# Performance work log

Measured on AMD Instinct MI355X. Metric: run time of the kernel, lower is better.

Reference implementation:

```python
import math
import jax, jax.numpy as jnp
import numpy as np

N, T, D, H = 256, 128, 1024, 1024


def setup_inputs() -> dict:
    key = jax.random.key(0)
    k1, k2, k3, k4, k5 = jax.random.split(key, 5)
    x = jax.random.normal(k1, (N, T, D), dtype=jnp.float32)
    A = jax.random.normal(k2, (N, H, 4, 4), dtype=jnp.float32)
    Wx = jax.random.normal(k3, (D, 4 * H), dtype=jnp.float32) / math.sqrt(D)
    Wh = jax.random.normal(k4, (H, 4 * H), dtype=jnp.float32) / math.sqrt(H)
    Wattn = jax.random.normal(k5, (H, 4 * H), dtype=jnp.float32) / math.sqrt(H)
    b = jnp.zeros((4 * H,), dtype=jnp.float32)
    return {"x": x, "A": A, "Wx": Wx, "Wh": Wh, "Wattn": Wattn, "b": b}


def reference(x, A, Wx, Wh, Wattn, b):
    n, t, d = x.shape
    h = A.shape[1]
    A_flat = A.reshape(n, h, -1)            # (N, H, 16)
    h0 = A_flat.mean(axis=-1)               # mean over 4x4 grid
    c0 = h0
    scale = 1.0 / math.sqrt(h)

    def step(carry, xt):
        prev_h, prev_c = carry
        # scaled dot-product attention over the 16 spatial locations
        scores = jnp.einsum('nh,nhl->nl', prev_h, A_flat) * scale  # (N, 16)
        w = jax.nn.softmax(scores, axis=1)
        attn = jnp.einsum('nhl,nl->nh', A_flat, w)                 # (N, H)
        pre = xt @ Wx + prev_h @ Wh + attn @ Wattn + b             # (N, 4H)
        ai, af, ao, ag = jnp.split(pre, 4, axis=1)
        i = jax.nn.sigmoid(ai)
        f = jax.nn.sigmoid(af)
        o = jax.nn.sigmoid(ao)
        g = jnp.tanh(ag)
        next_c = f * prev_c + i * g
        next_h = o * jnp.tanh(next_c)
        return (next_h, next_c), next_h

    xs = jnp.swapaxes(x, 0, 1)               # (T, N, D)
    _, hs = jax.lax.scan(step, (h0, c0), xs)  # hs: (T, N, H)
    return jnp.swapaxes(hs, 0, 1)             # (N, T, H)
```

## Files before the change

kernel.cpp:

```cpp
#include <hip/hip_runtime.h>
#include <hip/hip_bf16.h>
#include <stdint.h>

#define N_ 256
#define T_ 128
#define D_ 1024
#define H_ 1024
#define FH_ 4096
#define K2_ 2048

typedef __bf16 bf16x8 __attribute__((ext_vector_type(8)));
typedef float f32x4 __attribute__((ext_vector_type(4)));

__global__ __launch_bounds__(256) void transpose_cast(
    const float* __restrict__ src, int cols,
    __hip_bfloat16* __restrict__ dst, int dst_stride, int dst_coloff)
{
    __shared__ float tile[32][33];
    int cb = blockIdx.x * 32, rb = blockIdx.y * 32;
    int tx = threadIdx.x, ty = threadIdx.y;
#pragma unroll
    for (int i = 0; i < 4; i++)
        tile[ty + i * 8][tx] = src[(size_t)(rb + ty + i * 8) * cols + cb + tx];
    __syncthreads();
#pragma unroll
    for (int i = 0; i < 4; i++)
        dst[(size_t)(cb + ty + i * 8) * dst_stride + dst_coloff + rb + tx] =
            __float2bfloat16(tile[tx][ty + i * 8]);
}

#define BM 64
#define BN 128
#define BK 64
#define BKP 72

__global__ __launch_bounds__(256) void gemm_x(
    const float* __restrict__ Xf,
    const __hip_bfloat16* __restrict__ BT,
    __hip_bfloat16* __restrict__ Cp, int t0)
{
    __shared__ __hip_bfloat16 Al[BM][BKP];
    __shared__ __hip_bfloat16 Bl[BN][BKP];
    const int tid = threadIdx.x;
    const int lane = tid & 63, wid = tid >> 6;
    const int m0 = blockIdx.y * BM, n0 = blockIdx.x * BN;
    const int wm = (wid >> 1) * 32, wn = (wid & 1) * 64;
    const int rs = tid >> 3, kc = (tid & 7) * 8;
    f32x4 acc[2][4] = {};

    for (int k0 = 0; k0 < D_; k0 += BK) {
#pragma unroll
        for (int p = 0; p < BM; p += 32) {
            int r = rs + p;
            int g = m0 + r;
            int nn = g & 255, tl = g >> 8;
            const float* s = Xf + ((size_t)nn * T_ + (t0 + tl)) * D_ + k0 + kc;
            float4 v0 = *reinterpret_cast<const float4*>(s);
            float4 v1 = *reinterpret_cast<const float4*>(s + 4);
            __hip_bfloat16 h8[8];
            h8[0] = __float2bfloat16(v0.x); h8[1] = __float2bfloat16(v0.y);
            h8[2] = __float2bfloat16(v0.z); h8[3] = __float2bfloat16(v0.w);
            h8[4] = __float2bfloat16(v1.x); h8[5] = __float2bfloat16(v1.y);
            h8[6] = __float2bfloat16(v1.z); h8[7] = __float2bfloat16(v1.w);
            *reinterpret_cast<int4*>(&Al[r][kc]) = *reinterpret_cast<const int4*>(h8);
        }
#pragma unroll
        for (int p = 0; p < BN; p += 32) {
            int r = rs + p;
            const __hip_bfloat16* s = BT + (size_t)(n0 + r) * D_ + k0 + kc;
            *reinterpret_cast<int4*>(&Bl[r][kc]) = *reinterpret_cast<const int4*>(s);
        }
        __syncthreads();
        const int ko = (lane >> 4) * 8;
#pragma unroll
        for (int kk = 0; kk < BK; kk += 32) {
            bf16x8 a0 = *reinterpret_cast<const bf16x8*>(&Al[wm + (lane & 15)][kk + ko]);
            bf16x8 a1 = *reinterpret_cast<const bf16x8*>(&Al[wm + 16 + (lane & 15)][kk + ko]);
#pragma unroll
            for (int ni = 0; ni < 4; ni++) {
                bf16x8 bq = *reinterpret_cast<const bf16x8*>(&Bl[wn + ni * 16 + (lane & 15)][kk + ko]);
                acc[0][ni] = __builtin_amdgcn_mfma_f32_16x16x32_bf16(a0, bq, acc[0][ni], 0, 0, 0);
                acc[1][ni] = __builtin_amdgcn_mfma_f32_16x16x32_bf16(a1, bq, acc[1][ni], 0, 0, 0);
            }
        }
        __syncthreads();
    }
    const int cr = (lane >> 4) * 4, ccol = lane & 15;
#pragma unroll
    for (int mi = 0; mi < 2; mi++)
#pragma unroll
        for (int ni = 0; ni < 4; ni++)
#pragma unroll
            for (int r = 0; r < 4; r++) {
                size_t idx = (size_t)(m0 + wm + mi * 16 + cr + r) * FH_ + (n0 + wn + ni * 16 + ccol);
                Cp[idx] = __float2bfloat16(acc[mi][ni][r]);
            }
}

__global__ __launch_bounds__(256) void abf_cast(
    const float* __restrict__ A, __hip_bfloat16* __restrict__ Abf)
{
    size_t i = ((size_t)blockIdx.x * 256 + threadIdx.x) * 4;
    float4 v = *reinterpret_cast<const float4*>(A + i);
    __hip_bfloat16 o[4];
    o[0] = __float2bfloat16(v.x); o[1] = __float2bfloat16(v.y);
    o[2] = __float2bfloat16(v.z); o[3] = __float2bfloat16(v.w);
    *reinterpret_cast<uint2*>(Abf + i) = *reinterpret_cast<uint2*>(o);
}

__global__ __launch_bounds__(256) void init_p(
    const float* __restrict__ A, float* __restrict__ cbuf,
    __hip_bfloat16* __restrict__ hb0)
{
    const int n = blockIdx.x, tid = threadIdx.x;
    float hv[4];
#pragma unroll
    for (int q = 0; q < 4; q++) {
        const float4* Ap = reinterpret_cast<const float4*>(A + ((size_t)n * H_ + tid * 4 + q) * 16);
        float4 q0 = Ap[0], q1 = Ap[1], q2 = Ap[2], q3 = Ap[3];
        float s = q0.x + q0.y + q0.z + q0.w + q1.x + q1.y + q1.z + q1.w
                + q2.x + q2.y + q2.z + q2.w + q3.x + q3.y + q3.z + q3.w;
        hv[q] = s * 0.0625f;
    }
    *reinterpret_cast<float4*>(cbuf + (size_t)n * H_ + tid * 4) = *reinterpret_cast<float4*>(hv);
    __hip_bfloat16 h4[4];
#pragma unroll
    for (int q = 0; q < 4; q++) h4[q] = __float2bfloat16(hv[q]);
    *reinterpret_cast<uint2*>(hb0 + (size_t)n * K2_ + tid * 4) = *reinterpret_cast<uint2*>(h4);
}

__global__ __launch_bounds__(256) void wattn2(
    __hip_bfloat16* __restrict__ hbt,
    const __hip_bfloat16* __restrict__ Abf)
{
    __shared__ float red[4][16];
    const int n = blockIdx.x, tid = threadIdx.x;
    const int lane = tid & 63, wv4 = tid >> 6;

    float h4[4];
    {
        uint2 hraw = *reinterpret_cast<const uint2*>(hbt + (size_t)n * K2_ + tid * 4);
        __hip_bfloat16 hb4[4];
        *reinterpret_cast<uint2*>(hb4) = hraw;
#pragma unroll
        for (int q = 0; q < 4; q++) h4[q] = __bfloat162float(hb4[q]);
    }
    bf16x8 a[4][2];
    const __hip_bfloat16* ap = Abf + ((size_t)n * H_ + tid * 4) * 16;
#pragma unroll
    for (int q = 0; q < 4; q++) {
        a[q][0] = *reinterpret_cast<const bf16x8*>(ap + q * 16);
        a[q][1] = *reinterpret_cast<const bf16x8*>(ap + q * 16 + 8);
    }
    float spv[16];
#pragma unroll
    for (int l = 0; l < 8; l++) {
        spv[l]     = h4[0] * (float)a[0][0][l] + h4[1] * (float)a[1][0][l]
                   + h4[2] * (float)a[2][0][l] + h4[3] * (float)a[3][0][l];
        spv[l + 8] = h4[0] * (float)a[0][1][l] + h4[1] * (float)a[1][1][l]
                   + h4[2] * (float)a[2][1][l] + h4[3] * (float)a[3][1][l];
    }
#pragma unroll
    for (int l = 0; l < 16; l++) {
        spv[l] += __shfl_xor(spv[l], 1);  spv[l] += __shfl_xor(spv[l], 2);
        spv[l] += __shfl_xor(spv[l], 4);  spv[l] += __shfl_xor(spv[l], 8);
        spv[l] += __shfl_xor(spv[l], 16); spv[l] += __shfl_xor(spv[l], 32);
    }
    if (lane == 0) {
#pragma unroll
        for (int l = 0; l < 16; l++) red[wv4][l] = spv[l];
    }
    __syncthreads();
    float w[16], se = 0.f;
    {
        float sc[16], m;
#pragma unroll
        for (int l = 0; l < 16; l++)
            sc[l] = (red[0][l] + red[1][l] + red[2][l] + red[3][l]) * 0.03125f;
        m = sc[0];
#pragma unroll
        for (int l = 1; l < 16; l++) m = fmaxf(m, sc[l]);
#pragma unroll
        for (int l = 0; l < 16; l++) { w[l] = __expf(sc[l] - m); se += w[l]; }
        float inv = 1.f / se;
#pragma unroll
        for (int l = 0; l < 16; l++) w[l] *= inv;
    }
    __hip_bfloat16 o4[4];
#pragma unroll
    for (int q = 0; q < 4; q++) {
        float s = 0.f;
#pragma unroll
        for (int l = 0; l < 8; l++) s += w[l] * (float)a[q][0][l];
#pragma unroll
        for (int l = 0; l < 8; l++) s += w[l + 8] * (float)a[q][1][l];
        o4[q] = __float2bfloat16(s);
    }
    *reinterpret_cast<uint2*>(hbt + (size_t)n * K2_ + H_ + tid * 4) =
        *reinterpret_cast<uint2*>(o4);
}

#define LDAp 136

__global__ __launch_bounds__(512) void step_gemm(
    const __hip_bfloat16* __restrict__ hb_in,
    __hip_bfloat16* __restrict__ hb_out,
    const __hip_bfloat16* __restrict__ W2T,
    const __hip_bfloat16* __restrict__ xp,
    const float* __restrict__ bias,
    float* __restrict__ cbuf,
    float* __restrict__ out, int t)
{
    __shared__ __align__(16) char smem[69632];
    float* pls = (float*)smem;

    const int tid = threadIdx.x;
    const int lane = tid & 63, wv = tid >> 6;
    const int bid = blockIdx.x;
    const int q = bid >> 3;
    const int ct = (bid & 7) + 8 * (q >> 2);
    const int r  = q & 3;
    const int hc0 = ct * 16, n0 = r * 64;
    const int rs = tid >> 4;
    const int kc = (tid & 15) * 8;
    const int l15 = lane & 15, ko8 = (lane >> 4) * 8;
    const int wm = (wv >> 1) * 16, wn = (wv & 1) * 32;

    const int gB0 = ((rs) >> 4) * 1024 + hc0 + (rs & 15);
    const int gB1 = ((rs + 32) >> 4) * 1024 + hc0 + ((rs + 32) & 15);
    const __hip_bfloat16* aS0 = hb_in + (size_t)(n0 + rs) * K2_ + kc;
    const __hip_bfloat16* aS1 = hb_in + (size_t)(n0 + rs + 32) * K2_ + kc;
    const __hip_bfloat16* bS0 = W2T + (size_t)gB0 * K2_ + kc;
    const __hip_bfloat16* bS1 = W2T + (size_t)gB1 * K2_ + kc;

    int4 ra0, ra1, rb0, rb1;
    auto LOAD = [&](int k0) {
        ra0 = *reinterpret_cast<const int4*>(aS0 + k0);
        ra1 = *reinterpret_cast<const int4*>(aS1 + k0);
        rb0 = *reinterpret_cast<const int4*>(bS0 + k0);
        rb1 = *reinterpret_cast<const int4*>(bS1 + k0);
    };
    auto WRITE = [&](int b) {
        __hip_bfloat16* Al = (__hip_bfloat16*)(smem + b * 17408);
        __hip_bfloat16* Bl = (__hip_bfloat16*)(smem + 34816 + b * 17408);
        *reinterpret_cast<int4*>(Al + rs * LDAp + kc) = ra0;
        *reinterpret_cast<int4*>(Al + (rs + 32) * LDAp + kc) = ra1;
        *reinterpret_cast<int4*>(Bl + rs * LDAp + kc) = rb0;
        *reinterpret_cast<int4*>(Bl + (rs + 32) * LDAp + kc) = rb1;
    };

    LOAD(0);
    WRITE(0);
    __syncthreads();

    f32x4 acc0{}, acc1{};
#pragma unroll 1
    for (int it = 0; it < 16; ++it) {
        if (it < 15) LOAD((it + 1) * 128);
        const int cur = it & 1;
        const __hip_bfloat16* pA  = (const __hip_bfloat16*)(smem + cur * 17408) + (wm + l15) * LDAp + ko8;
        const __hip_bfloat16* pB0 = (const __hip_bfloat16*)(smem + 34816 + cur * 17408) + (wn + l15) * LDAp + ko8;
        const __hip_bfloat16* pB1 = pB0 + 16 * LDAp;
#pragma unroll
        for (int kf = 0; kf < 4; kf++) {
            bf16x8 af = *reinterpret_cast<const bf16x8*>(pA + kf * 32);
            bf16x8 b0 = *reinterpret_cast<const bf16x8*>(pB0 + kf * 32);
            bf16x8 b1 = *reinterpret_cast<const bf16x8*>(pB1 + kf * 32);
            acc0 = __builtin_amdgcn_mfma_f32_16x16x32_bf16(af, b0, acc0, 0, 0, 0);
            acc1 = __builtin_amdgcn_mfma_f32_16x16x32_bf16(af, b1, acc1, 0, 0, 0);
        }
        __syncthreads();
        if (it < 15) {
            WRITE(cur ^ 1);
            __syncthreads();
        }
    }

    {
        const int cr = (lane >> 4) * 4;
#pragma unroll
        for (int r4 = 0; r4 < 4; r4++) {
            pls[(wm + cr + r4) * 68 + wn + l15]      = acc0[r4];
            pls[(wm + cr + r4) * 68 + wn + 16 + l15] = acc1[r4];
        }
    }
    __syncthreads();

    {
        const int n_l = tid >> 3, c2 = (tid & 7) * 2;
        const int nn = n0 + n_l;
        float hv2[2], cv2[2];
        const size_t cbase = (size_t)nn * H_ + hc0 + c2;
        float2 cold = *reinterpret_cast<const float2*>(cbuf + cbase);
        cv2[0] = cold.x; cv2[1] = cold.y;
#pragma unroll
        for (int cc = 0; cc < 2; cc++) {
            const int c = c2 + cc;
            float pre[4];
#pragma unroll
            for (int s = 0; s < 4; s++) {
                const int gj = s * 1024 + hc0 + c;
                pre[s] = pls[n_l * 68 + s * 16 + c]
                       + __bfloat162float(xp[(size_t)nn * FH_ + gj]) + bias[gj];
            }
            float iv = 1.f / (1.f + __expf(-pre[0]));
            float fv = 1.f / (1.f + __expf(-pre[1]));
            float ov = 1.f / (1.f + __expf(-pre[2]));
            float gx = fminf(fmaxf(pre[3], -20.f), 20.f);
            float eg = __expf(2.f * gx);
            float gv = (eg - 1.f) / (eg + 1.f);
            float c2v = fv * cv2[cc] + iv * gv;
            cv2[cc] = c2v;
            float cx = fminf(fmaxf(c2v, -20.f), 20.f);
            float ec = __expf(2.f * cx);
            hv2[cc] = ov * (ec - 1.f) / (ec + 1.f);
        }
        *reinterpret_cast<float2*>(cbuf + cbase) = make_float2(cv2[0], cv2[1]);
        *reinterpret_cast<float2*>(out + ((size_t)nn * T_ + t) * H_ + hc0 + c2) =
            make_float2(hv2[0], hv2[1]);
        __hip_bfloat16 h2[2];
        h2[0] = __float2bfloat16(hv2[0]);
        h2[1] = __float2bfloat16(hv2[1]);
        *reinterpret_cast<uint32_t*>(hb_out + (size_t)nn * K2_ + hc0 + c2) =
            *reinterpret_cast<uint32_t*>(h2);
    }
}

extern "C" void kernel_launch(void* const* d_in, const int* in_sizes, int n_in,
                              void* d_out, int out_size, void* d_ws, size_t ws_size,
                              hipStream_t stream)
{
    const float* x     = (const float*)d_in[0];
    const float* A     = (const float*)d_in[1];
    const float* Wx    = (const float*)d_in[2];
    const float* Wh    = (const float*)d_in[3];
    const float* Wattn = (const float*)d_in[4];
    const float* b     = (const float*)d_in[5];
    float* out = (float*)d_out;
    char* ws = (char*)d_ws;
    dim3 tb(32, 8);

    const size_t SZ_W2T = (size_t)FH_ * K2_ * 2;
    const size_t SZ_WxT = (size_t)FH_ * D_ * 2;
    const size_t SZ_Abf = (size_t)N_ * H_ * 16 * 2;
    const size_t SZ_HB  = (size_t)N_ * K2_ * 2;
    const size_t SZ_C   = (size_t)N_ * H_ * 4;
    const size_t SZ_XPT = (size_t)N_ * FH_ * 2;

    size_t off = 0;
    __hip_bfloat16* W2T = (__hip_bfloat16*)(ws + off); off += SZ_W2T;
    __hip_bfloat16* WxT = (__hip_bfloat16*)(ws + off); off += SZ_WxT;
    __hip_bfloat16* Abf = (__hip_bfloat16*)(ws + off); off += SZ_Abf;
    __hip_bfloat16* hbA = (__hip_bfloat16*)(ws + off); off += SZ_HB;
    __hip_bfloat16* hbB = (__hip_bfloat16*)(ws + off); off += SZ_HB;
    float* cbuf = (float*)(ws + off); off += SZ_C;
    __hip_bfloat16* xpb = (__hip_bfloat16*)(ws + off);

    size_t rem = (ws_size > off) ? (ws_size - off) : 0;
    int TC = 64;
    while (TC > 1 && (size_t)TC * SZ_XPT > rem) TC >>= 1;

    transpose_cast<<<dim3(FH_ / 32, H_ / 32), tb, 0, stream>>>(Wh, FH_, W2T, K2_, 0);
    transpose_cast<<<dim3(FH_ / 32, H_ / 32), tb, 0, stream>>>(Wattn, FH_, W2T, K2_, H_);
    transpose_cast<<<dim3(FH_ / 32, D_ / 32), tb, 0, stream>>>(Wx, FH_, WxT, D_, 0);
    abf_cast<<<dim3((N_ * H_ * 16) / 1024), 256, 0, stream>>>(A, Abf);
    init_p<<<N_, 256, 0, stream>>>(A, cbuf, hbA);

    __hip_bfloat16* hbp[2] = {hbA, hbB};
    for (int t0 = 0; t0 < T_; t0 += TC) {
        int tc = (T_ - t0 < TC) ? (T_ - t0) : TC;
        gemm_x<<<dim3(FH_ / BN, tc * N_ / BM), 256, 0, stream>>>(x, WxT, xpb, t0);
        for (int tl = 0; tl < tc; tl++) {
            int t = t0 + tl;
            wattn2<<<N_, 256, 0, stream>>>(hbp[t & 1], Abf);
            step_gemm<<<dim3(256), 512, 0, stream>>>(
                hbp[t & 1], hbp[(t + 1) & 1], W2T,
                xpb + (size_t)tl * N_ * FH_, b, cbuf, out, t);
        }
    }
}
```

Before: 3.113 ms.

## Fuse attention and step GEMM into persistent kernel with grid barriers

Replaces the per-timestep pair of launches (attention kernel plus step GEMM) with one persistent kernel per time chunk. Blocks run the attention for one batch row, sync through a two-level atomic grid barrier, do the recurrent GEMM and LSTM update, then barrier again. The cell state stays in registers across steps, and the input-projection GEMM gets a remapped block order. This targets launch overhead and the DRAM round trip of c, at the cost of spin-wait barriers that need all 256 blocks co-resident, and a fixed chunk of 32 steps.

```diff
diff --git a/kernel.cpp b/kernel.cpp
--- a/kernel.cpp
+++ b/kernel.cpp
@@ -8,6 +8,7 @@
 #define H_ 1024
 #define FH_ 4096
 #define K2_ 2048
+#define TCHUNK 32
 
 typedef __bf16 bf16x8 __attribute__((ext_vector_type(8)));
 typedef float f32x4 __attribute__((ext_vector_type(4)));
@@ -43,7 +44,10 @@
     __shared__ __hip_bfloat16 Bl[BN][BKP];
     const int tid = threadIdx.x;
     const int lane = tid & 63, wid = tid >> 6;
-    const int m0 = blockIdx.y * BM, n0 = blockIdx.x * BN;
+    const int lin = blockIdx.y * gridDim.x + blockIdx.x;
+    const int cti = (lin & 7) + 8 * ((lin >> 3) & 3);
+    const int mti = lin >> 5;
+    const int m0 = mti * BM, n0 = cti * BN;
     const int wm = (wid >> 1) * 32, wn = (wid & 1) * 64;
     const int rs = tid >> 3, kc = (tid & 7) * 8;
     f32x4 acc[2][4] = {};
@@ -110,9 +114,10 @@
 
 __global__ __launch_bounds__(256) void init_p(
     const float* __restrict__ A, float* __restrict__ cbuf,
-    __hip_bfloat16* __restrict__ hb0)
+    __hip_bfloat16* __restrict__ hb0, unsigned* __restrict__ bar)
 {
     const int n = blockIdx.x, tid = threadIdx.x;
+    if (n == 0) { bar[tid] = 0u; bar[256 + tid] = 0u; }
     float hv[4];
 #pragma unroll
     for (int q = 0; q < 4; q++) {
@@ -129,94 +134,49 @@
     *reinterpret_cast<uint2*>(hb0 + (size_t)n * K2_ + tid * 4) = *reinterpret_cast<uint2*>(h4);
 }
 
-__global__ __launch_bounds__(256) void wattn2(
-    __hip_bfloat16* __restrict__ hbt,
-    const __hip_bfloat16* __restrict__ Abf)
-{
-    __shared__ float red[4][16];
-    const int n = blockIdx.x, tid = threadIdx.x;
-    const int lane = tid & 63, wv4 = tid >> 6;
-
-    float h4[4];
-    {
-        uint2 hraw = *reinterpret_cast<const uint2*>(hbt + (size_t)n * K2_ + tid * 4);
-        __hip_bfloat16 hb4[4];
-        *reinterpret_cast<uint2*>(hb4) = hraw;
-#pragma unroll
-        for (int q = 0; q < 4; q++) h4[q] = __bfloat162float(hb4[q]);
-    }
-    bf16x8 a[4][2];
-    const __hip_bfloat16* ap = Abf + ((size_t)n * H_ + tid * 4) * 16;
-#pragma unroll
-    for (int q = 0; q < 4; q++) {
-        a[q][0] = *reinterpret_cast<const bf16x8*>(ap + q * 16);
-        a[q][1] = *reinterpret_cast<const bf16x8*>(ap + q * 16 + 8);
-    }
-    float spv[16];
-#pragma unroll
-    for (int l = 0; l < 8; l++) {
-        spv[l]     = h4[0] * (float)a[0][0][l] + h4[1] * (float)a[1][0][l]
-                   + h4[2] * (float)a[2][0][l] + h4[3] * (float)a[3][0][l];
-        spv[l + 8] = h4[0] * (float)a[0][1][l] + h4[1] * (float)a[1][1][l]
-                   + h4[2] * (float)a[2][1][l] + h4[3] * (float)a[3][1][l];
-    }
-#pragma unroll
-    for (int l = 0; l < 16; l++) {
-        spv[l] += __shfl_xor(spv[l], 1);  spv[l] += __shfl_xor(spv[l], 2);
-        spv[l] += __shfl_xor(spv[l], 4);  spv[l] += __shfl_xor(spv[l], 8);
-        spv[l] += __shfl_xor(spv[l], 16); spv[l] += __shfl_xor(spv[l], 32);
-    }
-    if (lane == 0) {
-#pragma unroll
-        for (int l = 0; l < 16; l++) red[wv4][l] = spv[l];
+__device__ __forceinline__ void gridbar(unsigned* bar, int g)
+{
+    __syncthreads();
+    if (threadIdx.x == 0) {
+        __threadfence();
+        unsigned* leaf = bar + (g & 7) * 32;
+        unsigned* root = bar + 8 * 32;
+        unsigned* gen  = bar + 8 * 32 + 32;
+        unsigned tl = __hip_atomic_fetch_add(leaf, 1u, __ATOMIC_ACQ_REL, __HIP_MEMORY_SCOPE_AGENT);
+        unsigned r = tl >> 5;
+        if ((tl & 31u) == 31u) {
+            unsigned tr = __hip_atomic_fetch_add(root, 1u, __ATOMIC_ACQ_REL, __HIP_MEMORY_SCOPE_AGENT);
+            if ((tr & 7u) == 7u)
+                __hip_atomic_store(gen, r + 1u, __ATOMIC_RELEASE, __HIP_MEMORY_SCOPE_AGENT);
+        }
+        while (__hip_atomic_load(gen, __ATOMIC_ACQUIRE, __HIP_MEMORY_SCOPE_AGENT) < r + 1u)
+            __builtin_amdgcn_s_sleep(1);
+        __threadfence();
     }
     __syncthreads();
-    float w[16], se = 0.f;
-    {
-        float sc[16], m;
-#pragma unroll
-        for (int l = 0; l < 16; l++)
-            sc[l] = (red[0][l] + red[1][l] + red[2][l] + red[3][l]) * 0.03125f;
-        m = sc[0];
-#pragma unroll
-        for (int l = 1; l < 16; l++) m = fmaxf(m, sc[l]);
-#pragma unroll
-        for (int l = 0; l < 16; l++) { w[l] = __expf(sc[l] - m); se += w[l]; }
-        float inv = 1.f / se;
-#pragma unroll
-        for (int l = 0; l < 16; l++) w[l] *= inv;
-    }
-    __hip_bfloat16 o4[4];
-#pragma unroll
-    for (int q = 0; q < 4; q++) {
-        float s = 0.f;
-#pragma unroll
-        for (int l = 0; l < 8; l++) s += w[l] * (float)a[q][0][l];
-#pragma unroll
-        for (int l = 0; l < 8; l++) s += w[l + 8] * (float)a[q][1][l];
-        o4[q] = __float2bfloat16(s);
-    }
-    *reinterpret_cast<uint2*>(hbt + (size_t)n * K2_ + H_ + tid * 4) =
-        *reinterpret_cast<uint2*>(o4);
 }
 
 #define LDAp 136
 
-__global__ __launch_bounds__(512) void step_gemm(
-    const __hip_bfloat16* __restrict__ hb_in,
-    __hip_bfloat16* __restrict__ hb_out,
+__global__ __launch_bounds__(512) void persist3(
     const __hip_bfloat16* __restrict__ W2T,
-    const __hip_bfloat16* __restrict__ xp,
+    __hip_bfloat16* __restrict__ hbA,
+    __hip_bfloat16* __restrict__ hbB,
+    const __hip_bfloat16* __restrict__ xpb,
     const float* __restrict__ bias,
+    const __hip_bfloat16* __restrict__ Abf,
     float* __restrict__ cbuf,
-    float* __restrict__ out, int t)
-{
-    __shared__ __align__(16) char smem[69632];
+    float* __restrict__ out,
+    unsigned* __restrict__ bar,
+    int t0, int t1)
+{
+    __shared__ __align__(16) char smem[86016];
     float* pls = (float*)smem;
 
     const int tid = threadIdx.x;
     const int lane = tid & 63, wv = tid >> 6;
     const int bid = blockIdx.x;
+
     const int q = bid >> 3;
     const int ct = (bid & 7) + 8 * (q >> 2);
     const int r  = q & 3;
@@ -225,105 +185,176 @@
     const int kc = (tid & 15) * 8;
     const int l15 = lane & 15, ko8 = (lane >> 4) * 8;
     const int wm = (wv >> 1) * 16, wn = (wv & 1) * 32;
-
     const int gB0 = ((rs) >> 4) * 1024 + hc0 + (rs & 15);
     const int gB1 = ((rs + 32) >> 4) * 1024 + hc0 + ((rs + 32) & 15);
-    const __hip_bfloat16* aS0 = hb_in + (size_t)(n0 + rs) * K2_ + kc;
-    const __hip_bfloat16* aS1 = hb_in + (size_t)(n0 + rs + 32) * K2_ + kc;
     const __hip_bfloat16* bS0 = W2T + (size_t)gB0 * K2_ + kc;
     const __hip_bfloat16* bS1 = W2T + (size_t)gB1 * K2_ + kc;
 
-    int4 ra0, ra1, rb0, rb1;
-    auto LOAD = [&](int k0) {
-        ra0 = *reinterpret_cast<const int4*>(aS0 + k0);
-        ra1 = *reinterpret_cast<const int4*>(aS1 + k0);
-        rb0 = *reinterpret_cast<const int4*>(bS0 + k0);
-        rb1 = *reinterpret_cast<const int4*>(bS1 + k0);
-    };
-    auto WRITE = [&](int b) {
-        __hip_bfloat16* Al = (__hip_bfloat16*)(smem + b * 17408);
-        __hip_bfloat16* Bl = (__hip_bfloat16*)(smem + 34816 + b * 17408);
-        *reinterpret_cast<int4*>(Al + rs * LDAp + kc) = ra0;
-        *reinterpret_cast<int4*>(Al + (rs + 32) * LDAp + kc) = ra1;
-        *reinterpret_cast<int4*>(Bl + rs * LDAp + kc) = rb0;
-        *reinterpret_cast<int4*>(Bl + (rs + 32) * LDAp + kc) = rb1;
-    };
-
-    LOAD(0);
-    WRITE(0);
-    __syncthreads();
-
-    f32x4 acc0{}, acc1{};
+    const int n_l = tid >> 3, c2 = (tid & 7) * 2;
+    const int nn = n0 + n_l;
+    const size_t cbase = (size_t)nn * H_ + hc0 + c2;
+    float2 creg = *reinterpret_cast<const float2*>(cbuf + cbase);
+
+    for (int t = t0; t < t1; ++t) {
+        __hip_bfloat16* hcur = (t & 1) ? hbB : hbA;
+        __hip_bfloat16* hnxt = (t & 1) ? hbA : hbB;
+
+        {
+            float* red = (float*)smem;
+            float* wl  = (float*)smem + 128;
+            const int nA = bid;
+            uint32_t hraw = *reinterpret_cast<const uint32_t*>(
+                hcur + (size_t)nA * K2_ + tid * 2);
+            __hip_bfloat16 h2b[2];
+            *reinterpret_cast<uint32_t*>(h2b) = hraw;
+            float h0 = __bfloat162float(h2b[0]);
+            float h1 = __bfloat162float(h2b[1]);
+            const __hip_bfloat16* ap = Abf + ((size_t)nA * H_ + tid * 2) * 16;
+            bf16x8 a00 = *reinterpret_cast<const bf16x8*>(ap);
+            bf16x8 a01 = *reinterpret_cast<const bf16x8*>(ap + 8);
+            bf16x8 a10 = *reinterpret_cast<const bf16x8*>(ap + 16);
+            bf16x8 a11 = *reinterpret_cast<const bf16x8*>(ap + 24);
+            float spv[16];
+#pragma unroll
+            for (int l = 0; l < 8; l++) {
+                spv[l]     = h0 * (float)a00[l] + h1 * (float)a10[l];
+                spv[l + 8] = h0 * (float)a01[l] + h1 * (float)a11[l];
+            }
+#pragma unroll
+            for (int l = 0; l < 16; l++) {
+                spv[l] += __shfl_xor(spv[l], 1);  spv[l] += __shfl_xor(spv[l], 2);
+                spv[l] += __shfl_xor(spv[l], 4);  spv[l] += __shfl_xor(spv[l], 8);
+                spv[l] += __shfl_xor(spv[l], 16); spv[l] += __shfl_xor(spv[l], 32);
+            }
+            if (lane == 0) {
+#pragma unroll
+                for (int l = 0; l < 16; l++) red[wv * 16 + l] = spv[l];
+            }
+            __syncthreads();
+            if (tid < 16) {
+                float s = 0.f;
+#pragma unroll
+                for (int w8 = 0; w8 < 8; w8++) s += red[w8 * 16 + tid];
+                s *= 0.03125f;
+                float m = s;
+                m = fmaxf(m, __shfl_xor(m, 8)); m = fmaxf(m, __shfl_xor(m, 4));
+                m = fmaxf(m, __shfl_xor(m, 2)); m = fmaxf(m, __shfl_xor(m, 1));
+                float e = __expf(s - m);
+                float se = e;
+                se += __shfl_xor(se, 8); se += __shfl_xor(se, 4);
+                se += __shfl_xor(se, 2); se += __shfl_xor(se, 1);
+                wl[tid] = e / se;
+            }
+            __syncthreads();
+            float w[16];
+#pragma unroll
+            for (int l = 0; l < 16; l++) w[l] = wl[l];
+            float s0 = 0.f, s1 = 0.f;
+#pragma unroll
+            for (int l = 0; l < 8; l++) {
+                s0 += w[l] * (float)a00[l];  s0 += w[l + 8] * (float)a01[l];
+                s1 += w[l] * (float)a10[l];  s1 += w[l + 8] * (float)a11[l];
+            }
+            __hip_bfloat16 at2[2];
+            at2[0] = __float2bfloat16(s0);
+            at2[1] = __float2bfloat16(s1);
+            *reinterpret_cast<uint32_t*>(hcur + (size_t)nA * K2_ + H_ + tid * 2) =
+                *reinterpret_cast<uint32_t*>(at2);
+        }
+        gridbar(bar, bid);
+
+        const __hip_bfloat16* aS0 = hcur + (size_t)(n0 + rs) * K2_ + kc;
+        const __hip_bfloat16* aS1 = hcur + (size_t)(n0 + rs + 32) * K2_ + kc;
+        int4 ra0, ra1, rb0, rb1;
+        auto LOAD = [&](int k0) {
+            ra0 = *reinterpret_cast<const int4*>(aS0 + k0);
+            ra1 = *reinterpret_cast<const int4*>(aS1 + k0);
+            rb0 = *reinterpret_cast<const int4*>(bS0 + k0);
+            rb1 = *reinterpret_cast<const int4*>(bS1 + k0);
+        };
+        auto WRITE = [&](int b) {
+            __hip_bfloat16* Al = (__hip_bfloat16*)(smem + b * 17408);
+            __hip_bfloat16* Bl = (__hip_bfloat16*)(smem + 34816 + b * 17408);
+            *reinterpret_cast<int4*>(Al + rs * LDAp + kc) = ra0;
+            *reinterpret_cast<int4*>(Al + (rs + 32) * LDAp + kc) = ra1;
+            *reinterpret_cast<int4*>(Bl + rs * LDAp + kc) = rb0;
+            *reinterpret_cast<int4*>(Bl + (rs + 32) * LDAp + kc) = rb1;
+        };
+
+        LOAD(0);
+        WRITE(0);
+        __syncthreads();
+
+        f32x4 acc0{}, acc1{};
 #pragma unroll 1
-    for (int it = 0; it < 16; ++it) {
-        if (it < 15) LOAD((it + 1) * 128);
-        const int cur = it & 1;
-        const __hip_bfloat16* pA  = (const __hip_bfloat16*)(smem + cur * 17408) + (wm + l15) * LDAp + ko8;
-        const __hip_bfloat16* pB0 = (const __hip_bfloat16*)(smem + 34816 + cur * 17408) + (wn + l15) * LDAp + ko8;
-        const __hip_bfloat16* pB1 = pB0 + 16 * LDAp;
-#pragma unroll
-        for (int kf = 0; kf < 4; kf++) {
-            bf16x8 af = *reinterpret_cast<const bf16x8*>(pA + kf * 32);
-            bf16x8 b0 = *reinterpret_cast<const bf16x8*>(pB0 + kf * 32);
-            bf16x8 b1 = *reinterpret_cast<const bf16x8*>(pB1 + kf * 32);
-            acc0 = __builtin_amdgcn_mfma_f32_16x16x32_bf16(af, b0, acc0, 0, 0, 0);
-            acc1 = __builtin_amdgcn_mfma_f32_16x16x32_bf16(af, b1, acc1, 0, 0, 0);
+        for (int it = 0; it < 16; ++it) {
+            if (it < 15) LOAD((it + 1) * 128);
+            const int cur = it & 1;
+            const __hip_bfloat16* pA  = (const __hip_bfloat16*)(smem + cur * 17408) + (wm + l15) * LDAp + ko8;
+            const __hip_bfloat16* pB0 = (const __hip_bfloat16*)(smem + 34816 + cur * 17408) + (wn + l15) * LDAp + ko8;
+            const __hip_bfloat16* pB1 = pB0 + 16 * LDAp;
+#pragma unroll
+            for (int kf = 0; kf < 4; kf++) {
+                bf16x8 af = *reinterpret_cast<const bf16x8*>(pA + kf * 32);
+                bf16x8 b0 = *reinterpret_cast<const bf16x8*>(pB0 + kf * 32);
+                bf16x8 b1 = *reinterpret_cast<const bf16x8*>(pB1 + kf * 32);
+                acc0 = __builtin_amdgcn_mfma_f32_16x16x32_bf16(af, b0, acc0, 0, 0, 0);
+                acc1 = __builtin_amdgcn_mfma_f32_16x16x32_bf16(af, b1, acc1, 0, 0, 0);
+            }
+            __syncthreads();
+            if (it < 15) {
+                WRITE(cur ^ 1);
+                __syncthreads();
+            }
+        }
+
+        {
+            const int cr = (lane >> 4) * 4;
+#pragma unroll
+            for (int r4 = 0; r4 < 4; r4++) {
+                pls[(wm + cr + r4) * 68 + wn + l15]      = acc0[r4];
+                pls[(wm + cr + r4) * 68 + wn + 16 + l15] = acc1[r4];
+            }
         }
         __syncthreads();
-        if (it < 15) {
-            WRITE(cur ^ 1);
-            __syncthreads();
-        }
+
+        {
+            const __hip_bfloat16* xp = xpb + (size_t)(t - t0) * N_ * FH_;
+            float hv2[2], cv2[2] = {creg.x, creg.y};
+#pragma unroll
+            for (int cc = 0; cc < 2; cc++) {
+                const int c = c2 + cc;
+                float pre[4];
+#pragma unroll
+                for (int s = 0; s < 4; s++) {
+                    const int gj = s * 1024 + hc0 + c;
+                    pre[s] = pls[n_l * 68 + s * 16 + c]
+                           + __bfloat162float(xp[(size_t)nn * FH_ + gj]) + bias[gj];
+                }
+                float iv = 1.f / (1.f + __expf(-pre[0]));
+                float fv = 1.f / (1.f + __expf(-pre[1]));
+                float ov = 1.f / (1.f + __expf(-pre[2]));
+                float gx = fminf(fmaxf(pre[3], -20.f), 20.f);
+                float eg = __expf(2.f * gx);
+                float gv = (eg - 1.f) / (eg + 1.f);
+                float c2v = fv * cv2[cc] + iv * gv;
+                cv2[cc] = c2v;
+                float cx = fminf(fmaxf(c2v, -20.f), 20.f);
+                float ec = __expf(2.f * cx);
+                hv2[cc] = ov * (ec - 1.f) / (ec + 1.f);
+            }
+            creg = make_float2(cv2[0], cv2[1]);
+            *reinterpret_cast<float2*>(out + ((size_t)nn * T_ + t) * H_ + hc0 + c2) =
+                make_float2(hv2[0], hv2[1]);
+            __hip_bfloat16 h2[2];
+            h2[0] = __float2bfloat16(hv2[0]);
+            h2[1] = __float2bfloat16(hv2[1]);
+            *reinterpret_cast<uint32_t*>(hnxt + (size_t)nn * K2_ + hc0 + c2) =
+                *reinterpret_cast<uint32_t*>(h2);
+        }
+        gridbar(bar, bid);
     }
-
-    {
-        const int cr = (lane >> 4) * 4;
-#pragma unroll
-        for (int r4 = 0; r4 < 4; r4++) {
-            pls[(wm + cr + r4) * 68 + wn + l15]      = acc0[r4];
-            pls[(wm + cr + r4) * 68 + wn + 16 + l15] = acc1[r4];
-        }
-    }
-    __syncthreads();
-
-    {
-        const int n_l = tid >> 3, c2 = (tid & 7) * 2;
-        const int nn = n0 + n_l;
-        float hv2[2], cv2[2];
-        const size_t cbase = (size_t)nn * H_ + hc0 + c2;
-        float2 cold = *reinterpret_cast<const float2*>(cbuf + cbase);
-        cv2[0] = cold.x; cv2[1] = cold.y;
-#pragma unroll
-        for (int cc = 0; cc < 2; cc++) {
-            const int c = c2 + cc;
-            float pre[4];
-#pragma unroll
-            for (int s = 0; s < 4; s++) {
-                const int gj = s * 1024 + hc0 + c;
-                pre[s] = pls[n_l * 68 + s * 16 + c]
-                       + __bfloat162float(xp[(size_t)nn * FH_ + gj]) + bias[gj];
-            }
-            float iv = 1.f / (1.f + __expf(-pre[0]));
-            float fv = 1.f / (1.f + __expf(-pre[1]));
-            float ov = 1.f / (1.f + __expf(-pre[2]));
-            float gx = fminf(fmaxf(pre[3], -20.f), 20.f);
-            float eg = __expf(2.f * gx);
-            float gv = (eg - 1.f) / (eg + 1.f);
-            float c2v = fv * cv2[cc] + iv * gv;
-            cv2[cc] = c2v;
-            float cx = fminf(fmaxf(c2v, -20.f), 20.f);
-            float ec = __expf(2.f * cx);
-            hv2[cc] = ov * (ec - 1.f) / (ec + 1.f);
-        }
-        *reinterpret_cast<float2*>(cbuf + cbase) = make_float2(cv2[0], cv2[1]);
-        *reinterpret_cast<float2*>(out + ((size_t)nn * T_ + t) * H_ + hc0 + c2) =
-            make_float2(hv2[0], hv2[1]);
-        __hip_bfloat16 h2[2];
-        h2[0] = __float2bfloat16(hv2[0]);
-        h2[1] = __float2bfloat16(hv2[1]);
-        *reinterpret_cast<uint32_t*>(hb_out + (size_t)nn * K2_ + hc0 + c2) =
-            *reinterpret_cast<uint32_t*>(h2);
-    }
+    *reinterpret_cast<float2*>(cbuf + cbase) = creg;
 }
 
 extern "C" void kernel_launch(void* const* d_in, const int* in_sizes, int n_in,
@@ -345,7 +376,8 @@
     const size_t SZ_Abf = (size_t)N_ * H_ * 16 * 2;
     const size_t SZ_HB  = (size_t)N_ * K2_ * 2;
     const size_t SZ_C   = (size_t)N_ * H_ * 4;
-    const size_t SZ_XPT = (size_t)N_ * FH_ * 2;
+    const size_t SZ_BAR = 4096;
+    const size_t SZ_XPC = (size_t)TCHUNK * N_ * FH_ * 2;
 
     size_t off = 0;
     __hip_bfloat16* W2T = (__hip_bfloat16*)(ws + off); off += SZ_W2T;
@@ -353,29 +385,19 @@
     __hip_bfloat16* Abf = (__hip_bfloat16*)(ws + off); off += SZ_Abf;
     __hip_bfloat16* hbA = (__hip_bfloat16*)(ws + off); off += SZ_HB;
     __hip_bfloat16* hbB = (__hip_bfloat16*)(ws + off); off += SZ_HB;
-    float* cbuf = (float*)(ws + off); off += SZ_C;
+    float* cbuf   = (float*)(ws + off); off += SZ_C;
+    unsigned* bar = (unsigned*)(ws + off); off += SZ_BAR;
     __hip_bfloat16* xpb = (__hip_bfloat16*)(ws + off);
-
-    size_t rem = (ws_size > off) ? (ws_size - off) : 0;
-    int TC = 64;
-    while (TC > 1 && (size_t)TC * SZ_XPT > rem) TC >>= 1;
 
     transpose_cast<<<dim3(FH_ / 32, H_ / 32), tb, 0, stream>>>(Wh, FH_, W2T, K2_, 0);
     transpose_cast<<<dim3(FH_ / 32, H_ / 32), tb, 0, stream>>>(Wattn, FH_, W2T, K2_, H_);
     transpose_cast<<<dim3(FH_ / 32, D_ / 32), tb, 0, stream>>>(Wx, FH_, WxT, D_, 0);
     abf_cast<<<dim3((N_ * H_ * 16) / 1024), 256, 0, stream>>>(A, Abf);
-    init_p<<<N_, 256, 0, stream>>>(A, cbuf, hbA);
-
-    __hip_bfloat16* hbp[2] = {hbA, hbB};
-    for (int t0 = 0; t0 < T_; t0 += TC) {
-        int tc = (T_ - t0 < TC) ? (T_ - t0) : TC;
-        gemm_x<<<dim3(FH_ / BN, tc * N_ / BM), 256, 0, stream>>>(x, WxT, xpb, t0);
-        for (int tl = 0; tl < tc; tl++) {
-            int t = t0 + tl;
-            wattn2<<<N_, 256, 0, stream>>>(hbp[t & 1], Abf);
-            step_gemm<<<dim3(256), 512, 0, stream>>>(
-                hbp[t & 1], hbp[(t + 1) & 1], W2T,
-                xpb + (size_t)tl * N_ * FH_, b, cbuf, out, t);
-        }
+    init_p<<<N_, 256, 0, stream>>>(A, cbuf, hbA, bar);
+
+    for (int t0 = 0; t0 < T_; t0 += TCHUNK) {
+        gemm_x<<<dim3(FH_ / BN, TCHUNK * N_ / BM), 256, 0, stream>>>(x, WxT, xpb, t0);
+        persist3<<<dim3(256), 512, 0, stream>>>(
+            W2T, hbA, hbB, xpb, b, Abf, cbuf, out, bar, t0, t0 + TCHUNK);
     }
 }
```

Measured after the change: 9.623 ms. 3.09x slower.
